# Optimization experiments

Hardware: AMD Instinct MI355X
Metric: run time of the kernel (lower is better)

The kernel has to match this reference:

```python
import jax, jax.numpy as jnp
import numpy as np
import math

PERCENT = 0.5

def setup_inputs() -> dict:
    key = jax.random.key(0)
    x = jax.random.normal(key, (32, 128, 112, 112), dtype=jnp.float32)
    return {"x": x}

def reference(x):
    # x: [B, C, H, W]; per-pixel top-k over channels, keep values >= k-th largest, clamp at 0
    C = x.shape[1]
    k = math.ceil(PERCENT * C)
    xt = jnp.moveaxis(x, 1, -1)                 # [B, H, W, C]
    top_vals, _ = jax.lax.top_k(xt, k)          # [B, H, W, k]
    threshold = top_vals[..., -1:]              # k-th largest per pixel
    out = jnp.where(xt >= threshold, xt, jnp.float32(0.0))
    out = jnp.maximum(out, jnp.float32(0.0))    # clamp(min=0)
    return jnp.moveaxis(out, -1, 1)             # back to [B, C, H, W]
```

## Files before the change

### kernel.cpp

```cpp
#include <hip/hip_runtime.h>


#define CC   128
#define HWSZ 12544

__device__ __forceinline__ void bitonic64(float v[64]) {
  #pragma unroll
  for (int k = 2; k <= 64; k <<= 1) {
    #pragma unroll
    for (int j = k >> 1; j > 0; j >>= 1) {
      #pragma unroll
      for (int i = 0; i < 64; ++i) {
        int l = i ^ j;
        if (l > i) {
          float lo = fminf(v[i], v[l]);
          float hi = fmaxf(v[i], v[l]);
          bool up = ((i & k) == 0);
          v[i] = up ? lo : hi;
          v[l] = up ? hi : lo;
        }
      }
    }
  }
}

__global__ __launch_bounds__(256) void crelu_pct_kernel(
    const float* __restrict__ x, float* __restrict__ out) {
  const int t    = blockIdx.x * blockDim.x + threadIdx.x;
  const int q    = t >> 1;
  const int half = t & 1;
  const int n = q / HWSZ;
  const int p = q - n * HWSZ;
  const size_t base = (size_t)n * ((size_t)CC * HWSZ) + (size_t)p
                    + (size_t)(half << 6) * HWSZ;
  const float* xp = x + base;
  float*       op = out + base;

  float v[64];
  #pragma unroll
  for (int c = 0; c < 64; ++c) v[c] = xp[(size_t)c * HWSZ];
  bitonic64(v);

  float thr;
  {
    float mine  = half ? v[63] : v[0];
    float other = __shfl_xor(mine, 1, 64);
    thr = fmaxf(mine, other);
    #pragma unroll
    for (int i = 1; i < 64; ++i) {
      float m  = half ? v[63 - i] : v[i];
      float o  = __shfl_xor(m, 1, 64);
      thr = fminf(thr, fmaxf(m, o));
    }
  }

  #pragma unroll
  for (int c = 0; c < 64; ++c) {
    float w = xp[(size_t)c * HWSZ];
    op[(size_t)c * HWSZ] = (w >= thr && w > 0.0f) ? w : 0.0f;
  }
}

extern "C" void kernel_launch(void* const* d_in, const int* in_sizes, int n_in,
                              void* d_out, int out_size, void* d_ws, size_t ws_size,
                              hipStream_t stream) {
  const float* x = (const float*)d_in[0];
  float* out = (float*)d_out;
  const int npix = in_sizes[0] / CC;
  const int nthreads = npix * 2;
  const int block = 256;
  const int grid = nthreads / block;
  crelu_pct_kernel<<<grid, block, 0, stream>>>(x, out);
}
```

Baseline: 363.0 us.

## Split each pixel's channels across four lanes with cooperative bitonic merge

Each pixel's 128 channels are now handled by four threads of 32 channels each instead of two of 64. Every thread sorts its 32 values locally, in ascending or descending order depending on a sign flip. Partner lanes then merge through shuffle-based bitonic min/max steps to find the 64th-largest threshold. This cuts per-thread register pressure and sort work and doubles the thread count, aiming for more occupancy and better latency hiding on a memory-bound kernel. The cost is extra shuffle traffic and more complex merge logic.

Result: slower. 386.3 us (+6.4%).

```diff
diff --git a/kernel.cpp b/kernel.cpp
--- a/kernel.cpp
+++ b/kernel.cpp
@@ -4,13 +4,13 @@
 #define CC   128
 #define HWSZ 12544
 
-__device__ __forceinline__ void bitonic64(float v[64]) {
+__device__ __forceinline__ void bitonic32(float v[32]) {
   #pragma unroll
-  for (int k = 2; k <= 64; k <<= 1) {
+  for (int k = 2; k <= 32; k <<= 1) {
     #pragma unroll
     for (int j = k >> 1; j > 0; j >>= 1) {
       #pragma unroll
-      for (int i = 0; i < 64; ++i) {
+      for (int i = 0; i < 32; ++i) {
         int l = i ^ j;
         if (l > i) {
           float lo = fminf(v[i], v[l]);
@@ -26,36 +26,61 @@
 
 __global__ __launch_bounds__(256) void crelu_pct_kernel(
     const float* __restrict__ x, float* __restrict__ out) {
-  const int t    = blockIdx.x * blockDim.x + threadIdx.x;
-  const int q    = t >> 1;
-  const int half = t & 1;
+  const int t = blockIdx.x * blockDim.x + threadIdx.x;
+  const int q = t >> 2;
+  const int s = t & 3;
   const int n = q / HWSZ;
   const int p = q - n * HWSZ;
   const size_t base = (size_t)n * ((size_t)CC * HWSZ) + (size_t)p
-                    + (size_t)(half << 6) * HWSZ;
+                    + (size_t)(s << 5) * HWSZ;
   const float* xp = x + base;
   float*       op = out + base;
 
-  float v[64];
+  const unsigned smask = (s & 1) ? 0x80000000u : 0u;
+  const unsigned omask = smask ^ 0x80000000u;
+
+  float v[32];
   #pragma unroll
-  for (int c = 0; c < 64; ++c) v[c] = xp[(size_t)c * HWSZ];
-  bitonic64(v);
+  for (int c = 0; c < 32; ++c) {
+    float w = xp[(size_t)c * HWSZ];
+    v[c] = __uint_as_float(__float_as_uint(w) ^ smask);
+  }
+  bitonic32(v);
 
-  float thr;
-  {
-    float mine  = half ? v[63] : v[0];
-    float other = __shfl_xor(mine, 1, 64);
-    thr = fmaxf(mine, other);
+  #pragma unroll
+  for (int i = 0; i < 32; ++i) {
+    float r = __shfl_xor(v[i], 1, 64);
+    v[i] = fminf(v[i], -r);
+  }
+
+  #pragma unroll
+  for (int j = 16; j > 0; j >>= 1) {
     #pragma unroll
-    for (int i = 1; i < 64; ++i) {
-      float m  = half ? v[63 - i] : v[i];
-      float o  = __shfl_xor(m, 1, 64);
-      thr = fminf(thr, fmaxf(m, o));
+    for (int i = 0; i < 32; ++i) {
+      int l = i ^ j;
+      if (l > i) {
+        float lo = fminf(v[i], v[l]);
+        float hi = fmaxf(v[i], v[l]);
+        v[i] = lo;
+        v[l] = hi;
+      }
     }
   }
 
+  asm volatile("" ::: "memory");
+
+  float acc = __builtin_inff();
   #pragma unroll
-  for (int c = 0; c < 64; ++c) {
+  for (int u = 0; u < 32; ++u) {
+    float r = __shfl_xor(v[u], 3, 64);
+    float mine  = __uint_as_float(__float_as_uint(v[u]) ^ smask);
+    float other = __uint_as_float(__float_as_uint(r)    ^ omask);
+    acc = fminf(acc, fmaxf(mine, other));
+  }
+  const float thr = fminf(acc, __shfl_xor(acc, 1, 64));
+
+  #pragma unroll
+  for (int c = 0; c < 32; ++c) {
     float w = xp[(size_t)c * HWSZ];
     op[(size_t)c * HWSZ] = (w >= thr && w > 0.0f) ? w : 0.0f;
   }
@@ -67,7 +92,7 @@
   const float* x = (const float*)d_in[0];
   float* out = (float*)d_out;
   const int npix = in_sizes[0] / CC;
-  const int nthreads = npix * 2;
+  const int nthreads = npix * 4;
   const int block = 256;
   const int grid = nthreads / block;
   crelu_pct_kernel<<<grid, block, 0, stream>>>(x, out);
```
